# Performance work log

Hardware: AMD Instinct MI355X
Metric: run time of the kernel (lower is better)

Reference implementation:

```python
import jax, jax.numpy as jnp
import numpy as np

N = 50000
E = 800000
IN_C = 256
NHID = 32
HEADS = 4
OUT_C = 64
HID = NHID * HEADS  # 128
SLOPE = 0.2


def setup_inputs() -> dict:
    key = jax.random.key(0)
    ks = jax.random.split(key, 16)
    s = lambda *d: 1.0 / np.sqrt(d[0])
    inp = {
        "x": jax.random.normal(ks[0], (N, IN_C), dtype=jnp.float32),
        "edge_index": jax.random.randint(ks[1], (2, E), 0, N, dtype=jnp.int64),
        # conv1: GATConv(IN_C, NHID, heads=HEADS, concat=True)
        "W1": jax.random.normal(ks[2], (IN_C, HEADS * NHID), dtype=jnp.float32) * s(IN_C),
        "att_src1": jax.random.normal(ks[3], (HEADS, NHID), dtype=jnp.float32) * s(NHID),
        "att_dst1": jax.random.normal(ks[4], (HEADS, NHID), dtype=jnp.float32) * s(NHID),
        "b1": jnp.zeros((HEADS * NHID,), dtype=jnp.float32),
        # conv2: GATConv(HID, OUT_C, heads=1, concat=False)
        "W2": jax.random.normal(ks[5], (HID, OUT_C), dtype=jnp.float32) * s(HID),
        "att_src2": jax.random.normal(ks[6], (1, OUT_C), dtype=jnp.float32) * s(OUT_C),
        "att_dst2": jax.random.normal(ks[7], (1, OUT_C), dtype=jnp.float32) * s(OUT_C),
        "b2": jnp.zeros((OUT_C,), dtype=jnp.float32),
        # res1: Linear(IN_C, HID)
        "res1_w": jax.random.normal(ks[8], (IN_C, HID), dtype=jnp.float32) * s(IN_C),
        "res1_b": jnp.zeros((HID,), dtype=jnp.float32),
        # fc: Linear(HID, OUT_C)
        "fc_w": jax.random.normal(ks[9], (HID, OUT_C), dtype=jnp.float32) * s(HID),
        "fc_b": jnp.zeros((OUT_C,), dtype=jnp.float32),
    }
    return inp


def leaky_relu(x, slope=SLOPE):
    return jnp.where(x >= 0, x, slope * x)


def gat_conv(x, edge_index, W, att_src, att_dst, bias, heads, out_c, concat):
    """PyG GATConv with default add_self_loops=True, negative_slope=0.2."""
    n = x.shape[0]
    loop = jnp.arange(n, dtype=edge_index.dtype)
    src = jnp.concatenate([edge_index[0], loop])  # [E+N]
    dst = jnp.concatenate([edge_index[1], loop])
    h = (x @ W).reshape(n, heads, out_c)          # [N,H,C]
    a_src = (h * att_src[None]).sum(-1)           # [N,H]
    a_dst = (h * att_dst[None]).sum(-1)
    alpha = leaky_relu(a_src[src] + a_dst[dst])   # [E+N,H]
    # segment softmax over destination nodes (every node has a self loop)
    amax = jax.ops.segment_max(alpha, dst, num_segments=n)
    expa = jnp.exp(alpha - amax[dst])
    denom = jax.ops.segment_sum(expa, dst, num_segments=n)
    alpha = expa / (denom[dst] + 1e-16)
    msg = alpha[:, :, None] * h[src]              # [E+N,H,C] irregular gather
    out = jax.ops.segment_sum(msg, dst, num_segments=n)  # scatter-add
    if concat:
        out = out.reshape(n, heads * out_c)
    else:
        out = out.mean(axis=1)
    return out + bias


def reference(x, edge_index, W1, att_src1, att_dst1, b1, W2, att_src2, att_dst2, b2,
              res1_w, res1_b, fc_w, fc_b):
    x_res = x @ res1_w + res1_b
    h = gat_conv(x, edge_index, W1, att_src1, att_dst1, b1, HEADS, NHID, True) + x_res
    h_res = h @ fc_w + fc_b
    h = leaky_relu(h)
    z = gat_conv(h, edge_index, W2, att_src2, att_dst2, b2, 1, OUT_C, False) + h_res
    z = leaky_relu(z)
    return z
```

## Files before the change

kernel.cpp:

```cpp
#include <hip/hip_runtime.h>

typedef __attribute__((ext_vector_type(8))) short short8;
typedef __attribute__((ext_vector_type(4))) float f32x4;

constexpr int BCAP = 4096;

__device__ __forceinline__ ushort rne_bf16(float f) {
  uint u = __float_as_uint(f);
  uint r = (u + 0x7FFFu + ((u >> 16) & 1u)) >> 16;
  return (ushort)r;
}
__device__ __forceinline__ float bf16_lo(uint pair) { return __uint_as_float(pair << 16); }
__device__ __forceinline__ float bf16_hi(uint pair) { return __uint_as_float(pair & 0xffff0000u); }
__device__ __forceinline__ float bf1(ushort v) { return __uint_as_float((uint)v << 16); }
__device__ __forceinline__ float lrelu(float a) { return a >= 0.f ? a : 0.2f * a; }

__device__ __forceinline__ uint lrelu_pair(uint pair) {
  float lo = lrelu(bf16_lo(pair));
  float hi = lrelu(bf16_hi(pair));
  return (uint)rne_bf16(lo) | ((uint)rne_bf16(hi) << 16);
}
__device__ __forceinline__ float4 lrelu_bf8(float4 v) {
  uint4 u = *(uint4*)&v;
  u.x = lrelu_pair(u.x); u.y = lrelu_pair(u.y);
  u.z = lrelu_pair(u.z); u.w = lrelu_pair(u.w);
  return *(float4*)&u;
}
__device__ __forceinline__ float4 pack_bf8(float4 a, float4 b) {
  uint u0 = (uint)rne_bf16(a.x) | ((uint)rne_bf16(a.y) << 16);
  uint u1 = (uint)rne_bf16(a.z) | ((uint)rne_bf16(a.w) << 16);
  uint u2 = (uint)rne_bf16(b.x) | ((uint)rne_bf16(b.y) << 16);
  uint u3 = (uint)rne_bf16(b.z) | ((uint)rne_bf16(b.w) << 16);
  uint4 r; r.x = u0; r.y = u1; r.z = u2; r.w = u3;
  return *(float4*)&r;
}

__global__ __launch_bounds__(256) void prep_all_k(
    const int* __restrict__ ei, int E, int nEB,
    int* __restrict__ bcnt, uint2* __restrict__ tmp, int nbuck,
    const float* __restrict__ W1, const float* __restrict__ res1_w,
    const float* __restrict__ fc_w, const float* __restrict__ W2,
    ushort* __restrict__ Wt1, ushort* __restrict__ fcT, ushort* __restrict__ W2T)
{
  __shared__ int lcnt[400];
  __shared__ int gbase[400];
  const int tid = threadIdx.x, bid = blockIdx.x;
  const long gstride = (long)gridDim.x * 256;
  const long g0 = (long)bid * 256 + tid;

  if (bid < nEB) {
    for (int i = tid; i < nbuck; i += 256) lcnt[i] = 0;
    __syncthreads();
    const int ebase = bid * 4096;
    int srcs[16], dsts[16], rk[16];
#pragma unroll
    for (int i = 0; i < 16; ++i) {
      int e = ebase + i * 256 + tid;
      if (e < E) {
        srcs[i] = ei[e];
        dsts[i] = ei[E + e];
        rk[i] = atomicAdd(&lcnt[dsts[i] >> 7], 1);
      } else dsts[i] = -1;
    }
    __syncthreads();
    for (int b = tid; b < nbuck; b += 256)
      gbase[b] = lcnt[b] ? atomicAdd(&bcnt[b], lcnt[b]) : 0;
    __syncthreads();
#pragma unroll
    for (int i = 0; i < 16; ++i) {
      if (dsts[i] >= 0) {
        int b = dsts[i] >> 7;
        tmp[(size_t)b * BCAP + gbase[b] + rk[i]] = make_uint2((uint)srcs[i], (uint)dsts[i]);
      }
    }
  }

  for (long gi = g0; gi < 81920; gi += gstride) {
    const float* src; ushort* dst; int K, NO; long local;
    if (gi < 32768)            { src = W1;     dst = Wt1;          K = 256; NO = 128; local = gi; }
    else if (gi < 65536)       { src = res1_w; dst = Wt1 + 32768;  K = 256; NO = 128; local = gi - 32768; }
    else if (gi < 65536+8192)  { src = fc_w;   dst = fcT;          K = 128; NO = 64;  local = gi - 65536; }
    else                       { src = W2;     dst = W2T;          K = 128; NO = 64;  local = gi - 65536 - 8192; }
    int n = (int)(local / K), k = (int)(local % K);
    dst[local] = rne_bf16(src[(size_t)k * NO + n]);
  }
}

__global__ __launch_bounds__(512) void scan_buckets_k(const int* __restrict__ bcnt,
                                                      int* __restrict__ bbase,
                                                      int* __restrict__ offp,
                                                      int nbuck, int N) {
  __shared__ int sh[512];
  int tid = threadIdx.x;
  int v = (tid < nbuck) ? bcnt[tid] : 0;
  sh[tid] = v;
  __syncthreads();
  for (int o = 1; o < 512; o <<= 1) {
    int t = (tid >= o) ? sh[tid - o] : 0;
    __syncthreads();
    sh[tid] += t;
    __syncthreads();
  }
  if (tid < nbuck) bbase[tid] = sh[tid] - v;
  if (tid == nbuck - 1) { bbase[nbuck] = sh[tid]; offp[N] = sh[tid]; }
}

__global__ __launch_bounds__(512) void gemm1_k(
    const float* __restrict__ x, const ushort* __restrict__ Wt1,
    const float* __restrict__ res1_b,
    const float* __restrict__ att_s1, const float* __restrict__ att_d1,
    ushort* __restrict__ h1bf, ushort* __restrict__ xresbf,
    float* __restrict__ a_s, float* __restrict__ a_d,
    const uint2* __restrict__ tmp, const int* __restrict__ bcnt,
    const int* __restrict__ bbase, int* __restrict__ offp,
    int* __restrict__ csr, int nbuck, int M)
{
  constexpr int LDA = 72;
  __shared__ ushort smem[64 * LDA + 256 * LDA];
  const int bid = blockIdx.x, tid = threadIdx.x;
  ushort* As = smem;
  ushort* Bs = smem + 64 * LDA;
  const int w = tid >> 6, l = tid & 63;
  const int wr = w >> 2, wc = w & 3;
  const int l15 = l & 15, lg = l >> 4;
  const int row0 = bid * 64;
  const int srow = tid >> 3, sch = tid & 7;

  int gra = row0 + srow; if (gra >= M) gra = M - 1;
  const float*  Apf = x + (size_t)gra * 256 + sch * 8;
  const ushort* Bp  = Wt1 + (size_t)srow * 256 + sch * 8;

  f32x4 acc[2][4] = {};
  float4 raCa, raCb, rbC0, rbC1, rbC2, rbC3;
  float4 raNa, raNb, rbN0, rbN1, rbN2, rbN3;
  raCa = *(const float4*)(Apf);
  raCb = *(const float4*)(Apf + 4);
  rbC0 = *(const float4*)(Bp);
  rbC1 = *(const float4*)(Bp + 64 * 256);
  rbC2 = *(const float4*)(Bp + 128 * 256);
  rbC3 = *(const float4*)(Bp + 192 * 256);

#pragma unroll
  for (int kt = 0; kt < 4; ++kt) {
    __syncthreads();
    *(float4*)&As[srow * LDA + sch * 8] = pack_bf8(raCa, raCb);
    *(float4*)&Bs[(0 * 64 + srow) * LDA + sch * 8] = rbC0;
    *(float4*)&Bs[(1 * 64 + srow) * LDA + sch * 8] = rbC1;
    *(float4*)&Bs[(2 * 64 + srow) * LDA + sch * 8] = rbC2;
    *(float4*)&Bs[(3 * 64 + srow) * LDA + sch * 8] = rbC3;
    __syncthreads();
    if (kt < 3) {
      int k1 = (kt + 1) * 64;
      raNa = *(const float4*)(Apf + k1);
      raNb = *(const float4*)(Apf + k1 + 4);
      rbN0 = *(const float4*)(Bp + k1);
      rbN1 = *(const float4*)(Bp + 64 * 256 + k1);
      rbN2 = *(const float4*)(Bp + 128 * 256 + k1);
      rbN3 = *(const float4*)(Bp + 192 * 256 + k1);
    }
    short8 aF[2][2], bF[4][2];
#pragma unroll
    for (int m = 0; m < 2; ++m)
#pragma unroll
      for (int kk = 0; kk < 2; ++kk)
        aF[m][kk] = *(const short8*)&As[(wr * 32 + m * 16 + l15) * LDA + kk * 32 + lg * 8];
#pragma unroll
    for (int n = 0; n < 4; ++n)
#pragma unroll
      for (int kk = 0; kk < 2; ++kk)
        bF[n][kk] = *(const short8*)&Bs[(wc * 64 + n * 16 + l15) * LDA + kk * 32 + lg * 8];
#pragma unroll
    for (int m = 0; m < 2; ++m)
#pragma unroll
      for (int n = 0; n < 4; ++n)
#pragma unroll
        for (int kk = 0; kk < 2; ++kk)
          acc[m][n] = __builtin_amdgcn_mfma_f32_16x16x32_bf16(aF[m][kk], bF[n][kk], acc[m][n], 0, 0, 0);
    raCa = raNa; raCb = raNb;
    rbC0 = rbN0; rbC1 = rbN1; rbC2 = rbN2; rbC3 = rbN3;
  }
  __syncthreads();

  ushort* Cs = smem;
#pragma unroll
  for (int m = 0; m < 2; ++m)
#pragma unroll
    for (int n = 0; n < 4; ++n)
#pragma unroll
      for (int j = 0; j < 4; ++j) {
        int rl = wr * 32 + m * 16 + lg * 4 + j;
        int col = wc * 64 + n * 16 + l15;
        float v = acc[m][n][j] + (col >= 128 ? res1_b[col - 128] : 0.f);
        Cs[rl * 256 + col] = rne_bf16(v);
      }
  __syncthreads();

  {
    int r = tid >> 3, s = tid & 7, h = s >> 1;
    int gr = row0 + r;
    float ps = 0.f, pd = 0.f;
#pragma unroll
    for (int i = 0; i < 16; ++i) {
      int col = s * 16 + i;
      float v = bf1(Cs[r * 256 + col]);
      ps += v * att_s1[h * 32 + (col & 31)];
      pd += v * att_d1[h * 32 + (col & 31)];
    }
    ps += __shfl_xor(ps, 1, 64);
    pd += __shfl_xor(pd, 1, 64);
    if (!(s & 1) && gr < M) { a_s[gr * 4 + h] = ps; a_d[gr * 4 + h] = pd; }
  }

#pragma unroll
  for (int idx = tid; idx < 2048; idx += 512) {
    int row = idx >> 5, c16 = idx & 31;
    int gr = row0 + row;
    if (gr < M) {
      uint4 v = *(const uint4*)&Cs[row * 256 + c16 * 8];
      if (c16 < 16) *(uint4*)&h1bf[(size_t)gr * 128 + c16 * 8] = v;
      else          *(uint4*)&xresbf[(size_t)gr * 128 + (c16 - 16) * 8] = v;
    }
  }

  if (bid < nbuck) {
    __syncthreads();
    int* lcnt = (int*)smem;
    int* excl = lcnt + 128;
    const int vbase = bid * 128;
    const int nloc = ((vbase + 128 < M) ? 128 : M - vbase);
    const int cntb = bcnt[bid];
    const int bbase0 = bbase[bid];
    const uint2* bt = tmp + (size_t)bid * BCAP;
    if (tid < 128) lcnt[tid] = 0;
    __syncthreads();
    for (int e = tid; e < cntb; e += 512)
      atomicAdd(&lcnt[(int)bt[e].y - vbase], 1);
    __syncthreads();
    if (tid < 128) {
      int v = lcnt[tid];
      int sc = v;
#pragma unroll
      for (int o = 1; o < 64; o <<= 1) {
        int t = __shfl_up(sc, o, 64);
        if ((tid & 63) >= o) sc += t;
      }
      excl[tid] = sc - v;
    }
    __syncthreads();
    if (tid >= 64 && tid < 128) excl[tid] += excl[63] + lcnt[63];
    __syncthreads();
    if (tid < nloc) offp[vbase + tid] = bbase0 + excl[tid];
    if (tid < 128) lcnt[tid] = 0;
    __syncthreads();
    for (int e = tid; e < cntb; e += 512) {
      uint2 t = bt[e];
      int li = (int)t.y - vbase;
      int r = atomicAdd(&lcnt[li], 1);
      csr[bbase0 + excl[li] + r] = (int)t.x;
    }
  }
}

__global__ __launch_bounds__(512) void gemm2_k(
    const ushort* __restrict__ hpre,
    const ushort* __restrict__ fcT,
    const float* __restrict__ fc_b,
    const float* __restrict__ att_s2, const float* __restrict__ att_d2,
    ushort* __restrict__ hresb, ushort* __restrict__ h2bf,
    float* __restrict__ a_s, float* __restrict__ a_d, int M)
{
  constexpr int LDA = 72;
  __shared__ ushort smem[64 * LDA + 64 * LDA];
  const int tid = threadIdx.x, y = blockIdx.y;
  const ushort* B = fcT + (size_t)y * 64 * 128;
  ushort* out = y ? h2bf : hresb;
  const int row0 = blockIdx.x * 64;
  ushort* As = smem;
  ushort* Bs = smem + 64 * LDA;
  const int w = tid >> 6, l = tid & 63;
  const int wr = w >> 1, wc = w & 1;
  const int l15 = l & 15, lg = l >> 4;
  const int srow = tid >> 3, sch = tid & 7;

  int gra = row0 + srow; if (gra >= M) gra = M - 1;
  const ushort* Ap = hpre + (size_t)gra * 128 + sch * 8;
  const ushort* Bp = B + (size_t)srow * 128 + sch * 8;

  f32x4 acc[2] = {};
  float4 raC = *(const float4*)(Ap);
  float4 rbC = *(const float4*)(Bp);
  if (y) raC = lrelu_bf8(raC);
  float4 raN, rbN;

#pragma unroll
  for (int kt = 0; kt < 2; ++kt) {
    __syncthreads();
    *(float4*)&As[srow * LDA + sch * 8] = raC;
    *(float4*)&Bs[srow * LDA + sch * 8] = rbC;
    __syncthreads();
    if (kt < 1) {
      raN = *(const float4*)(Ap + 64);
      rbN = *(const float4*)(Bp + 64);
      if (y) raN = lrelu_bf8(raN);
    }

    short8 aF[2], bF[2][2];
#pragma unroll
    for (int kk = 0; kk < 2; ++kk)
      aF[kk] = *(const short8*)&As[(wr * 16 + l15) * LDA + kk * 32 + lg * 8];
#pragma unroll
    for (int n = 0; n < 2; ++n)
#pragma unroll
      for (int kk = 0; kk < 2; ++kk)
        bF[n][kk] = *(const short8*)&Bs[(wc * 32 + n * 16 + l15) * LDA + kk * 32 + lg * 8];
#pragma unroll
    for (int n = 0; n < 2; ++n)
#pragma unroll
      for (int kk = 0; kk < 2; ++kk)
        acc[n] = __builtin_amdgcn_mfma_f32_16x16x32_bf16(aF[kk], bF[n][kk], acc[n], 0, 0, 0);
    raC = raN; rbC = rbN;
  }
  __syncthreads();

  ushort* Cs = smem;
#pragma unroll
  for (int n = 0; n < 2; ++n)
#pragma unroll
    for (int j = 0; j < 4; ++j) {
      int rl = wr * 16 + lg * 4 + j;
      int col = wc * 32 + n * 16 + l15;
      float v = acc[n][j] + (y == 0 ? fc_b[col] : 0.f);
      Cs[rl * 64 + col] = rne_bf16(v);
    }
  __syncthreads();

  if (y == 1) {
    int r = tid >> 3, s = tid & 7;
    int gr = row0 + r;
    float ps = 0.f, pd = 0.f;
#pragma unroll
    for (int i = 0; i < 8; ++i) {
      int col = s * 8 + i;
      float v = bf1(Cs[r * 64 + col]);
      ps += v * att_s2[col];
      pd += v * att_d2[col];
    }
    ps += __shfl_xor(ps, 1, 64); pd += __shfl_xor(pd, 1, 64);
    ps += __shfl_xor(ps, 2, 64); pd += __shfl_xor(pd, 2, 64);
    ps += __shfl_xor(ps, 4, 64); pd += __shfl_xor(pd, 4, 64);
    if (s == 0 && gr < M) { a_s[gr] = ps; a_d[gr] = pd; }
  }

  {
    int row = tid >> 3, c16 = tid & 7;
    int gr = row0 + row;
    if (gr < M)
      *(uint4*)&out[(size_t)gr * 64 + c16 * 8] = *(const uint4*)&Cs[row * 64 + c16 * 8];
  }
}

__global__ __launch_bounds__(256) void aggr1_k(const uint* __restrict__ h1u,
                                               const uint* __restrict__ xresu,
                                               const float* __restrict__ a_s,
                                               const float* __restrict__ a_d,
                                               const int* __restrict__ off,
                                               const int* __restrict__ csr,
                                               const float* __restrict__ b1,
                                               uint* __restrict__ hpreu, int n) {
  int w = threadIdx.x >> 6, l = threadIdx.x & 63;
  int d = blockIdx.x * 4 + w;
  if (d >= n) return;
  int h = l >> 4, c = l * 2;
  int le = l & 15, hb = l & 48;
  float adh = a_d[d * 4 + h];
  float ws = __expf(lrelu(a_s[d * 4 + h] + adh));
  uint pd = h1u[(size_t)d * 64 + l];
  float lsum = ws, accx = ws * bf16_lo(pd), accy = ws * bf16_hi(pd);

  int s0 = off[d], s1 = off[d + 1];
  int p = s0;
  for (; p + 16 <= s1; p += 16) {
    int idxv = csr[p + le];
    float wv = __expf(lrelu(a_s[idxv * 4 + h] + adh));
    float wi[16]; int sv[16];
#pragma unroll
    for (int i = 0; i < 16; ++i) {
      wi[i] = __shfl(wv, hb + i, 64);
      sv[i] = __shfl(idxv, i, 64);
    }
#pragma unroll
    for (int i = 0; i < 16; ++i) {
      uint q = h1u[(size_t)sv[i] * 64 + l];
      lsum += wi[i];
      accx += wi[i] * bf16_lo(q);
      accy += wi[i] * bf16_hi(q);
    }
  }
  if (p < s1) {
    int rem = s1 - p;
    int jp = p + le;
    bool valid = jp < s1;
    int jc = valid ? jp : s1 - 1;
    int idxv = csr[jc];
    float wv = valid ? __expf(lrelu(a_s[idxv * 4 + h] + adh)) : 0.f;
    for (int i = 0; i < rem; i += 4) {
#pragma unroll
      for (int j = 0; j < 4; ++j) {
        float wib = __shfl(wv, hb + i + j, 64);
        int svb = __shfl(idxv, i + j, 64);
        uint q = h1u[(size_t)svb * 64 + l];
        lsum += wib;
        accx += wib * bf16_lo(q);
        accy += wib * bf16_hi(q);
      }
    }
  }
  float inv = 1.f / (lsum + 1e-16f);
  uint xr = xresu[(size_t)d * 64 + l];
  float vx = accx * inv + b1[c] + bf16_lo(xr);
  float vy = accy * inv + b1[c + 1] + bf16_hi(xr);
  hpreu[(size_t)d * 64 + l] = (uint)rne_bf16(vx) | ((uint)rne_bf16(vy) << 16);
}

__global__ __launch_bounds__(256) void aggr2_k(const ushort* __restrict__ h2b,
                                               const ushort* __restrict__ hresb,
                                               const float* __restrict__ a_s,
                                               const float* __restrict__ a_d,
                                               const int* __restrict__ off,
                                               const int* __restrict__ csr,
                                               const float* __restrict__ b2,
                                               float* __restrict__ out, int n) {
  int w = threadIdx.x >> 6, l = threadIdx.x & 63;
  int d = blockIdx.x * 4 + w;
  if (d >= n) return;
  int le = l & 15;
  float adh = a_d[d];
  float ws = __expf(lrelu(a_s[d] + adh));
  float lsum = ws;
  float acc = ws * bf1(h2b[(size_t)d * 64 + l]);

  int s0 = off[d], s1 = off[d + 1];
  int p = s0;
  for (; p + 16 <= s1; p += 16) {
    int idxv = csr[p + le];
    float wv = __expf(lrelu(a_s[idxv] + adh));
    float wi[16]; int sv[16];
#pragma unroll
    for (int i = 0; i < 16; ++i) {
      wi[i] = __shfl(wv, i, 64);
      sv[i] = __shfl(idxv, i, 64);
    }
#pragma unroll
    for (int i = 0; i < 16; ++i) {
      float fv = bf1(h2b[(size_t)sv[i] * 64 + l]);
      lsum += wi[i];
      acc += wi[i] * fv;
    }
  }
  if (p < s1) {
    int rem = s1 - p;
    int jp = p + le;
    bool valid = jp < s1;
    int jc = valid ? jp : s1 - 1;
    int idxv = csr[jc];
    float wv = valid ? __expf(lrelu(a_s[idxv] + adh)) : 0.f;
    for (int i = 0; i < rem; i += 4) {
#pragma unroll
      for (int j = 0; j < 4; ++j) {
        float wib = __shfl(wv, i + j, 64);
        int svb = __shfl(idxv, i + j, 64);
        float fv = bf1(h2b[(size_t)svb * 64 + l]);
        lsum += wib;
        acc += wib * fv;
      }
    }
  }
  float inv = 1.f / (lsum + 1e-16f);
  float z = acc * inv + b2[l] + bf1(hresb[(size_t)d * 64 + l]);
  out[(size_t)d * 64 + l] = lrelu(z);
}

extern "C" void kernel_launch(void* const* d_in, const int* in_sizes, int n_in,
                              void* d_out, int out_size, void* d_ws, size_t ws_size,
                              hipStream_t stream) {
  const float* x        = (const float*)d_in[0];
  const int*   ei       = (const int*)d_in[1];
  const float* W1       = (const float*)d_in[2];
  const float* att_src1 = (const float*)d_in[3];
  const float* att_dst1 = (const float*)d_in[4];
  const float* b1       = (const float*)d_in[5];
  const float* W2       = (const float*)d_in[6];
  const float* att_src2 = (const float*)d_in[7];
  const float* att_dst2 = (const float*)d_in[8];
  const float* b2       = (const float*)d_in[9];
  const float* res1_w   = (const float*)d_in[10];
  const float* res1_b   = (const float*)d_in[11];
  const float* fc_w     = (const float*)d_in[12];
  const float* fc_b     = (const float*)d_in[13];
  float* out = (float*)d_out;

  const int N = in_sizes[0] / 256;
  const int E = in_sizes[1] / 2;
  const int nbuck = (N + 127) / 128;
  const int nEB = (E + 4095) / 4096;

  ushort* h1bf   = (ushort*)d_ws;
  ushort* xresbf = h1bf + (size_t)N * 128;
  uint*   hpreu  = (uint*)(xresbf + (size_t)N * 128);
  float*  as1    = (float*)(hpreu + (size_t)N * 64);
  float*  ad1    = as1 + (size_t)N * 4;
  ushort* Wt1    = (ushort*)(ad1 + (size_t)N * 4);
  ushort* fcT    = Wt1 + 256 * 256;
  ushort* W2T    = fcT + 64 * 128;
  int* offp      = (int*)(W2T + 64 * 128);
  int* csr       = offp + N + 1;
  int* bcnt      = csr + E;
  int* bbase     = bcnt + 512;
  uint2* tmp     = (uint2*)(((uintptr_t)(bbase + 520) + 7) & ~(uintptr_t)7);
  ushort* h2bf   = h1bf;
  ushort* hresb  = xresbf;
  float*  as2 = as1, *ad2 = ad1;

  const int ngemm = (N + 63) / 64;

  hipMemsetAsync(bcnt, 0, 512 * 4, stream);
  prep_all_k<<<nEB, 256, 0, stream>>>(ei, E, nEB, bcnt, tmp, nbuck,
                                      W1, res1_w, fc_w, W2, Wt1, fcT, W2T);
  scan_buckets_k<<<1, 512, 0, stream>>>(bcnt, bbase, offp, nbuck, N);

  gemm1_k<<<ngemm, 512, 0, stream>>>(x, Wt1, res1_b, att_src1, att_dst1,
                                     h1bf, xresbf, as1, ad1,
                                     tmp, bcnt, bbase, offp, csr, nbuck, N);

  aggr1_k<<<(N + 3) / 4, 256, 0, stream>>>((const uint*)h1bf, (const uint*)xresbf, as1, ad1,
                                           offp, csr, b1, hpreu, N);

  gemm2_k<<<dim3(ngemm, 2), 512, 0, stream>>>(
      (const ushort*)hpreu, fcT, fc_b,
      att_src2, att_dst2, hresb, h2bf, as2, ad2, N);

  aggr2_k<<<(N + 3) / 4, 256, 0, stream>>>(h2bf, hresb, as2, ad2, offp, csr, b2, out, N);
}
```

Before: 153.7 us.

## Stage full A tile in LDS once and read W fragments directly from global

```diff
diff --git a/kernel.cpp b/kernel.cpp
--- a/kernel.cpp
+++ b/kernel.cpp
@@ -115,81 +115,62 @@
     const int* __restrict__ bbase, int* __restrict__ offp,
     int* __restrict__ csr, int nbuck, int M)
 {
-  constexpr int LDA = 72;
-  __shared__ ushort smem[64 * LDA + 256 * LDA];
+  constexpr int LDA = 264;
+  __shared__ ushort smem[64 * LDA];
   const int bid = blockIdx.x, tid = threadIdx.x;
-  ushort* As = smem;
-  ushort* Bs = smem + 64 * LDA;
   const int w = tid >> 6, l = tid & 63;
-  const int wr = w >> 2, wc = w & 3;
+  const int wc = w;
   const int l15 = l & 15, lg = l >> 4;
   const int row0 = bid * 64;
-  const int srow = tid >> 3, sch = tid & 7;
-
-  int gra = row0 + srow; if (gra >= M) gra = M - 1;
-  const float*  Apf = x + (size_t)gra * 256 + sch * 8;
-  const ushort* Bp  = Wt1 + (size_t)srow * 256 + sch * 8;
-
-  f32x4 acc[2][4] = {};
-  float4 raCa, raCb, rbC0, rbC1, rbC2, rbC3;
-  float4 raNa, raNb, rbN0, rbN1, rbN2, rbN3;
-  raCa = *(const float4*)(Apf);
-  raCb = *(const float4*)(Apf + 4);
-  rbC0 = *(const float4*)(Bp);
-  rbC1 = *(const float4*)(Bp + 64 * 256);
-  rbC2 = *(const float4*)(Bp + 128 * 256);
-  rbC3 = *(const float4*)(Bp + 192 * 256);
-
+
+  {
+    int row = tid >> 3, seg = tid & 7;
+    int gr = row0 + row; if (gr >= M) gr = M - 1;
+    const float* xp = x + (size_t)gr * 256 + seg * 32;
+#pragma unroll
+    for (int it = 0; it < 4; ++it) {
+      float4 a = *(const float4*)(xp + it * 8);
+      float4 b = *(const float4*)(xp + it * 8 + 4);
+      *(float4*)&smem[row * LDA + seg * 32 + it * 8] = pack_bf8(a, b);
+    }
+  }
+  __syncthreads();
+
+  f32x4 acc[4][2] = {};
+  const ushort* Bw = Wt1 + ((size_t)wc * 32 + l15) * 256 + lg * 8;
 #pragma unroll
   for (int kt = 0; kt < 4; ++kt) {
-    __syncthreads();
-    *(float4*)&As[srow * LDA + sch * 8] = pack_bf8(raCa, raCb);
-    *(float4*)&Bs[(0 * 64 + srow) * LDA + sch * 8] = rbC0;
-    *(float4*)&Bs[(1 * 64 + srow) * LDA + sch * 8] = rbC1;
-    *(float4*)&Bs[(2 * 64 + srow) * LDA + sch * 8] = rbC2;
-    *(float4*)&Bs[(3 * 64 + srow) * LDA + sch * 8] = rbC3;
-    __syncthreads();
-    if (kt < 3) {
-      int k1 = (kt + 1) * 64;
-      raNa = *(const float4*)(Apf + k1);
-      raNb = *(const float4*)(Apf + k1 + 4);
-      rbN0 = *(const float4*)(Bp + k1);
-      rbN1 = *(const float4*)(Bp + 64 * 256 + k1);
-      rbN2 = *(const float4*)(Bp + 128 * 256 + k1);
-      rbN3 = *(const float4*)(Bp + 192 * 256 + k1);
-    }
-    short8 aF[2][2], bF[4][2];
-#pragma unroll
-    for (int m = 0; m < 2; ++m)
+    const int k0 = kt * 64;
+    short8 aF[4][2], bF[2][2];
+#pragma unroll
+    for (int n = 0; n < 2; ++n)
 #pragma unroll
       for (int kk = 0; kk < 2; ++kk)
-        aF[m][kk] = *(const short8*)&As[(wr * 32 + m * 16 + l15) * LDA + kk * 32 + lg * 8];
-#pragma unroll
-    for (int n = 0; n < 4; ++n)
+        bF[n][kk] = *(const short8*)(Bw + (size_t)(n * 16) * 256 + k0 + kk * 32);
+#pragma unroll
+    for (int m = 0; m < 4; ++m)
 #pragma unroll
       for (int kk = 0; kk < 2; ++kk)
-        bF[n][kk] = *(const short8*)&Bs[(wc * 64 + n * 16 + l15) * LDA + kk * 32 + lg * 8];
-#pragma unroll
-    for (int m = 0; m < 2; ++m)
-#pragma unroll
-      for (int n = 0; n < 4; ++n)
+        aF[m][kk] = *(const short8*)&smem[(m * 16 + l15) * LDA + k0 + kk * 32 + lg * 8];
+#pragma unroll
+    for (int m = 0; m < 4; ++m)
+#pragma unroll
+      for (int n = 0; n < 2; ++n)
 #pragma unroll
         for (int kk = 0; kk < 2; ++kk)
           acc[m][n] = __builtin_amdgcn_mfma_f32_16x16x32_bf16(aF[m][kk], bF[n][kk], acc[m][n], 0, 0, 0);
-    raCa = raNa; raCb = raNb;
-    rbC0 = rbN0; rbC1 = rbN1; rbC2 = rbN2; rbC3 = rbN3;
   }
   __syncthreads();
 
   ushort* Cs = smem;
 #pragma unroll
-  for (int m = 0; m < 2; ++m)
-#pragma unroll
-    for (int n = 0; n < 4; ++n)
+  for (int m = 0; m < 4; ++m)
+#pragma unroll
+    for (int n = 0; n < 2; ++n)
 #pragma unroll
       for (int j = 0; j < 4; ++j) {
-        int rl = wr * 32 + m * 16 + lg * 4 + j;
-        int col = wc * 64 + n * 16 + l15;
+        int rl = m * 16 + lg * 4 + j;
+        int col = wc * 32 + n * 16 + l15;
         float v = acc[m][n][j] + (col >= 128 ? res1_b[col - 128] : 0.f);
         Cs[rl * 256 + col] = rne_bf16(v);
       }
```

Measured after the change: 161.5 us. +5.1%, slower.
